# Performance work log

Hardware: AMD Instinct MI355X
Metric: run time of the kernel (lower is better)

The kernel has to match this reference:

```python
import jax, jax.numpy as jnp
import numpy as np

N = 50000      # nodes
E = 800000     # edges (avg degree 16)
DIN = 128      # input_dim
H = 256        # hidden_channels
DOUT = 64      # output_dim


def _glorot(k, shape):
    lim = float(np.sqrt(6.0 / (shape[0] + shape[1])))
    return jax.random.uniform(k, shape, jnp.float32, -lim, lim)


def setup_inputs() -> dict:
    key = jax.random.key(0)
    ks = jax.random.split(key, 10)
    return {
        "x": jax.random.normal(ks[0], (N, DIN), jnp.float32),
        "W1": _glorot(ks[3], (DIN, H)), "b1": jnp.zeros((H,), jnp.float32),
        "W2": _glorot(ks[4], (H, H)),   "b2": jnp.zeros((H,), jnp.float32),
        "L1w": _glorot(ks[5], (H, DIN)), "L1b": jnp.zeros((DIN,), jnp.float32),
        "L2w": _glorot(ks[6], (DIN, H)), "L2b": jnp.zeros((H,), jnp.float32),
        "W3": _glorot(ks[7], (H, DOUT)), "b3": jnp.zeros((DOUT,), jnp.float32),
        "adj": jax.random.randint(ks[1], (2, E), 0, N),
        "adj2": jax.random.randint(ks[2], (2, E), 0, N),
        "mode": 1,  # 1 -> 'l' (return logits); 0 -> softmax over classes
    }


def gcn_conv(x, edge_index, W, b):
    """PyG-style GCNConv: add self-loops, symmetric D^-1/2 A D^-1/2 norm,
    aggregate neighbor features, then (here fused) linear transform."""
    n = x.shape[0]
    loop = jnp.arange(n)
    src = jnp.concatenate([edge_index[0], loop])  # message sources (j)
    dst = jnp.concatenate([edge_index[1], loop])  # aggregation targets (i)
    deg = jax.ops.segment_sum(jnp.ones(src.shape[0], x.dtype), dst, num_segments=n)
    dinv = jax.lax.rsqrt(jnp.maximum(deg, 1.0))   # deg >= 1 due to self-loops
    norm = dinv[src] * dinv[dst]                  # [E+N]
    h = x @ W                                     # transform first (smaller of the two dims either way)
    msg = h[src] * norm[:, None]                  # gather + scale, [E+N, out]
    return jax.ops.segment_sum(msg, dst, num_segments=n) + b


def reference(x, W1, b1, W2, b2, L1w, L1b, L2w, L2b, W3, b3, adj, adj2, mode):
    h = jax.nn.relu(gcn_conv(x, adj, W1, b1))      # GCNConv(in->h) on adj
    h = jax.nn.relu(gcn_conv(h, adj2, W2, b2))     # GCNConv(h->h) on adj2
    h = jax.nn.relu(h @ L1w + L1b)                 # Linear(h->in)
    h = jax.nn.relu(h @ L2w + L2b)                 # Linear(in->h)
    out = gcn_conv(h, adj2, W3, b3)                # GCNConv(h->out) on adj2
    # dropout has p=0 -> identity
    return out if mode == 1 else jax.nn.softmax(out, axis=1)
```

## Files before the change

kernel.cpp:

```cpp
#include <hip/hip_runtime.h>
#include <hip/hip_bf16.h>
#include <cstdint>
#include <cstddef>

#define NNODES 50000
#define NEDGES 800000
#define D_IN   128
#define D_H    256
#define D_OUT  64
#define SCAN_BS 256
#define SCAN_NB ((NNODES + SCAN_BS - 1) / SCAN_BS)
#define BSH    9
#define BKN    (1 << BSH)
#define NBKT   ((NNODES + BKN - 1) / BKN)
#define MAXB   12288
#define CHUNK  2048

typedef __attribute__((ext_vector_type(8))) short bf16x8;
typedef __attribute__((ext_vector_type(4))) float f32x4;

__device__ __forceinline__ unsigned short f2bf(float f) {
    unsigned u = __builtin_bit_cast(unsigned, f);
    unsigned r = (u + 0x7FFFu + ((u >> 16) & 1u)) >> 16;
    return (unsigned short)r;
}
__device__ __forceinline__ float bf2f(unsigned short h) {
    unsigned u = ((unsigned)h) << 16;
    return __builtin_bit_cast(float, u);
}


__global__ __launch_bounds__(256) void k_bin(const int* __restrict__ adjA, const int* __restrict__ adjB,
                                             int* __restrict__ bcnt, unsigned* __restrict__ binned, int e) {
    __shared__ int h[NBKT], pfx[NBKT], put[NBKT], gbase[NBKT];
    __shared__ unsigned stage[CHUNK];
    const int g = blockIdx.y;
    const int* srcp = g ? adjB : adjA;
    const int* dstp = srcp + e;
    unsigned* outp = binned + (size_t)g * NBKT * MAXB;
    int* bc = bcnt + g * NBKT;
    const int tid = threadIdx.x;
    const int base = blockIdx.x * CHUNK;
    const int nrem = min(CHUNK, e - base);
    if (nrem <= 0) return;

    for (int t = tid; t < NBKT; t += 256) { h[t] = 0; put[t] = 0; }
    __syncthreads();

    unsigned pv[8];
    int bv[8];
    #pragma unroll
    for (int q = 0; q < 8; ++q) {
        int i = base + q * 256 + tid;
        bv[q] = -1;
        if (i < e) {
            int s = srcp[i];
            int d = dstp[i];
            pv[q] = ((unsigned)d << 16) | (unsigned)s;
            bv[q] = d >> BSH;
            atomicAdd(&h[bv[q]], 1);
        }
    }
    __syncthreads();
    if (tid == 0) {
        int r = 0;
        for (int k = 0; k < NBKT; ++k) { pfx[k] = r; r += h[k]; }
    }
    __syncthreads();
    #pragma unroll
    for (int q = 0; q < 8; ++q) {
        if (bv[q] >= 0) {
            int p = pfx[bv[q]] + atomicAdd(&put[bv[q]], 1);
            stage[p] = pv[q];
        }
    }
    __syncthreads();
    if (tid < NBKT && h[tid] > 0) gbase[tid] = atomicAdd(&bc[tid], h[tid]);
    __syncthreads();
    for (int idx = tid; idx < nrem; idx += 256) {
        unsigned v = stage[idx];
        int bb = v >> (16 + BSH);
        outp[(size_t)bb * MAXB + gbase[bb] + (idx - pfx[bb])] = v;
    }
}

__global__ __launch_bounds__(256) void k_hist_b(const unsigned* __restrict__ binned, const int* __restrict__ bcnt,
                                                int* __restrict__ cnt1, int* __restrict__ cnt2, int n) {
    __shared__ int lc[BKN];
    const int g = blockIdx.y;
    const int b = blockIdx.x;
    const unsigned* in = binned + (size_t)g * NBKT * MAXB + (size_t)b * MAXB;
    int* cnt = g ? cnt2 : cnt1;
    const int nb = bcnt[g * NBKT + b];
    const int base = b << BSH;
    for (int t = threadIdx.x; t < BKN; t += 256) lc[t] = 0;
    __syncthreads();
    for (int t = threadIdx.x; t < nb; t += 256) {
        unsigned v = in[t];
        atomicAdd(&lc[(v >> 16) & (BKN - 1)], 1);
    }
    __syncthreads();
    for (int t = threadIdx.x; t < BKN; t += 256)
        if (base + t < n) cnt[base + t] = lc[t];
}

__global__ __launch_bounds__(256) void k_scan_local2(const int* __restrict__ cnt1, const int* __restrict__ cnt2,
                                                     int* __restrict__ rp1, int* __restrict__ rp2,
                                                     int* __restrict__ bsum, int n) {
    __shared__ int s[SCAN_BS];
    const int g = blockIdx.x / SCAN_NB;
    const int blk = blockIdx.x - g * SCAN_NB;
    const int* cnt = g ? cnt2 : cnt1;
    int* rp = g ? rp2 : rp1;
    int t = threadIdx.x;
    int i = blk * SCAN_BS + t;
    int v = (i < n) ? cnt[i] : 0;
    int sum = v;
    s[t] = v;
    __syncthreads();
    #pragma unroll
    for (int off = 1; off < SCAN_BS; off <<= 1) {
        int u = (t >= off) ? s[t - off] : 0;
        __syncthreads();
        sum += u;
        s[t] = sum;
        __syncthreads();
    }
    if (i < n) rp[i] = sum - v;
    if (t == SCAN_BS - 1) bsum[blockIdx.x] = sum;
}

__global__ __launch_bounds__(256) void k_scan_top2(int* __restrict__ bsum) {
    __shared__ int s[SCAN_BS];
    int* b = bsum + blockIdx.x * SCAN_NB;
    int t = threadIdx.x;
    int v = (t < SCAN_NB) ? b[t] : 0;
    int sum = v;
    s[t] = v;
    __syncthreads();
    #pragma unroll
    for (int off = 1; off < SCAN_BS; off <<= 1) {
        int u = (t >= off) ? s[t - off] : 0;
        __syncthreads();
        sum += u;
        s[t] = sum;
        __syncthreads();
    }
    if (t < SCAN_NB) b[t] = sum - v;
}

__global__ __launch_bounds__(256) void k_scan_add2(int* __restrict__ rp1, int* __restrict__ rp2,
                                                   const int* __restrict__ bsum, int n) {
    const int g = blockIdx.x / SCAN_NB;
    const int blk = blockIdx.x - g * SCAN_NB;
    int* rp = g ? rp2 : rp1;
    int i = blk * SCAN_BS + threadIdx.x;
    if (i < n) rp[i] += bsum[blockIdx.x];
    if (i == 0) rp[n] = NEDGES;
}

__global__ void k_dinv2x(const int* __restrict__ cnt1, const int* __restrict__ cnt2,
                         float* __restrict__ dinv1, float* __restrict__ dinv2, int n) {
    int i = blockIdx.x * blockDim.x + threadIdx.x;
    if (i < n) dinv1[i] = rsqrtf((float)(cnt1[i] + 1));
    else if (i < 2 * n) dinv2[i - n] = rsqrtf((float)(cnt2[i - n] + 1));
}

__global__ __launch_bounds__(256) void k_scatter_lds(const unsigned* __restrict__ binned, const int* __restrict__ bcnt,
                                                     const int* __restrict__ rp1, const int* __restrict__ rp2,
                                                     int* __restrict__ col1, int* __restrict__ col2, int n) {
    __shared__ int lcur[BKN];
    __shared__ int srt[MAXB];
    const int g = blockIdx.y;
    const int b = blockIdx.x;
    const unsigned* in = binned + (size_t)g * NBKT * MAXB + (size_t)b * MAXB;
    const int* rp = g ? rp2 : rp1;
    int* col = g ? col2 : col1;
    const int base = b << BSH;
    const int rpb = rp[base];
    const int nb = bcnt[g * NBKT + b];
    for (int t = threadIdx.x; t < BKN; t += 256) {
        int node = base + t;
        lcur[t] = (node < n) ? rp[node] - rpb : 0;
    }
    __syncthreads();
    for (int t = threadIdx.x; t < nb; t += 256) {
        unsigned v = in[t];
        int pos = atomicAdd(&lcur[(v >> 16) & (BKN - 1)], 1);
        srt[pos] = (int)(v & 0xFFFFu);
    }
    __syncthreads();
    for (int t = threadIdx.x; t < nb; t += 256) col[rpb + t] = srt[t];
}


template<int F, bool PRESCALE>
__global__ __launch_bounds__(256) void k_quant(const float* __restrict__ in, const float* __restrict__ dscale,
                                               short* __restrict__ q, float* __restrict__ qs, int n) {
    constexpr int VPT = F / 64;
    const int lane = threadIdx.x & 63;
    const int i = blockIdx.x * 4 + (threadIdx.x >> 6);
    if (i >= n) return;
    float v[VPT];
    const float* p = in + (size_t)i * F + lane * VPT;
    if constexpr (VPT == 4) { float4 t = *(const float4*)p; v[0] = t.x; v[1] = t.y; v[2] = t.z; v[3] = t.w; }
    else if constexpr (VPT == 2) { float2 t = *(const float2*)p; v[0] = t.x; v[1] = t.y; }
    else v[0] = *p;
    if constexpr (PRESCALE) {
        float d = dscale[i];
        #pragma unroll
        for (int c = 0; c < VPT; ++c) v[c] *= d;
    }
    float m = 0.f;
    #pragma unroll
    for (int c = 0; c < VPT; ++c) m = fmaxf(m, fabsf(v[c]));
    #pragma unroll
    for (int off = 32; off > 0; off >>= 1) m = fmaxf(m, __shfl_xor(m, off));
    float inv = (m > 0.f) ? 32767.0f / m : 0.f;
    short* qp = q + (size_t)i * F + lane * VPT;
    if constexpr (VPT == 4) {
        short4 o;
        o.x = (short)__float2int_rn(v[0] * inv);
        o.y = (short)__float2int_rn(v[1] * inv);
        o.z = (short)__float2int_rn(v[2] * inv);
        o.w = (short)__float2int_rn(v[3] * inv);
        *(short4*)qp = o;
    } else if constexpr (VPT == 2) {
        short2 o;
        o.x = (short)__float2int_rn(v[0] * inv);
        o.y = (short)__float2int_rn(v[1] * inv);
        *(short2*)qp = o;
    } else {
        *qp = (short)__float2int_rn(v[0] * inv);
    }
    if (lane == 0) qs[i] = m * (1.0f / 32767.0f);
}


template<int F, int OUTM>
__global__ __launch_bounds__(256) void k_agg3(const short* __restrict__ q, const float* __restrict__ qs,
                                              const int* __restrict__ rp, const int* __restrict__ col,
                                              const float* __restrict__ dinv, const float* __restrict__ bias,
                                              void* __restrict__ outv, int n) {
    constexpr int VPT = F / 64;
    const int lane = threadIdx.x & 63;
    const int i = blockIdx.x * 4 + (threadIdx.x >> 6);
    if (i >= n) return;
    const short* ql = q + lane * VPT;
    float acc[VPT];
    #pragma unroll
    for (int c = 0; c < VPT; ++c) acc[c] = 0.f;

    int k = rp[i], end = rp[i + 1];

    auto body1 = [&](int j) {
        float s = qs[j];
        const short* pj = ql + (size_t)j * F;
        if constexpr (VPT == 4) {
            short4 v = *(const short4*)pj;
            acc[0] += s * (float)v.x; acc[1] += s * (float)v.y;
            acc[2] += s * (float)v.z; acc[3] += s * (float)v.w;
        } else if constexpr (VPT == 2) {
            short2 v = *(const short2*)pj;
            acc[0] += s * (float)v.x; acc[1] += s * (float)v.y;
        } else {
            acc[0] += s * (float)(*pj);
        }
    };

    body1(i);
    for (; k + 4 <= end; k += 4) {
        int j0 = col[k], j1 = col[k + 1], j2 = col[k + 2], j3 = col[k + 3];
        float s0 = qs[j0], s1 = qs[j1], s2 = qs[j2], s3 = qs[j3];
        if constexpr (VPT == 4) {
            short4 v0 = *(const short4*)(ql + (size_t)j0 * F);
            short4 v1 = *(const short4*)(ql + (size_t)j1 * F);
            short4 v2 = *(const short4*)(ql + (size_t)j2 * F);
            short4 v3 = *(const short4*)(ql + (size_t)j3 * F);
            acc[0] += s0 * (float)v0.x + s1 * (float)v1.x + s2 * (float)v2.x + s3 * (float)v3.x;
            acc[1] += s0 * (float)v0.y + s1 * (float)v1.y + s2 * (float)v2.y + s3 * (float)v3.y;
            acc[2] += s0 * (float)v0.z + s1 * (float)v1.z + s2 * (float)v2.z + s3 * (float)v3.z;
            acc[3] += s0 * (float)v0.w + s1 * (float)v1.w + s2 * (float)v2.w + s3 * (float)v3.w;
        } else if constexpr (VPT == 2) {
            short2 v0 = *(const short2*)(ql + (size_t)j0 * F);
            short2 v1 = *(const short2*)(ql + (size_t)j1 * F);
            short2 v2 = *(const short2*)(ql + (size_t)j2 * F);
            short2 v3 = *(const short2*)(ql + (size_t)j3 * F);
            acc[0] += s0 * (float)v0.x + s1 * (float)v1.x + s2 * (float)v2.x + s3 * (float)v3.x;
            acc[1] += s0 * (float)v0.y + s1 * (float)v1.y + s2 * (float)v2.y + s3 * (float)v3.y;
        } else {
            float v0 = (float)ql[(size_t)j0 * F];
            float v1 = (float)ql[(size_t)j1 * F];
            float v2 = (float)ql[(size_t)j2 * F];
            float v3 = (float)ql[(size_t)j3 * F];
            acc[0] += s0 * v0 + s1 * v1 + s2 * v2 + s3 * v3;
        }
    }
    for (; k < end; ++k) body1(col[k]);

    float di = dinv[i];
    if constexpr (OUTM == 0) {
        unsigned short* o = (unsigned short*)outv + (size_t)i * 2 * F + lane * VPT;
        #pragma unroll
        for (int c = 0; c < VPT; ++c) {
            float val = acc[c] * di;
            unsigned short h = f2bf(val);
            unsigned short l = f2bf(val - bf2f(h));
            o[c] = h;
            o[F + c] = l;
        }
    } else {
        float* o = (float*)outv + (size_t)i * F + lane * VPT;
        #pragma unroll
        for (int c = 0; c < VPT; ++c) o[c] = acc[c] * di + bias[lane * VPT + c];
    }
}


__device__ __forceinline__ void wconv1(const float* __restrict__ W, unsigned short* __restrict__ Th,
                                       unsigned short* __restrict__ Tl, int idx, int K, int Nc) {
    int k = idx / Nc, n = idx - k * Nc;
    float v = W[idx];
    unsigned short h = f2bf(v);
    unsigned short l = f2bf(v - bf2f(h));
    Th[(size_t)n * K + k] = h;
    Tl[(size_t)n * K + k] = l;
}

__global__ void k_wconv_all(const float* W1, const float* W2, const float* L1w, const float* L2w, const float* W3,
                            unsigned short* W1h, unsigned short* W1l, unsigned short* W2h, unsigned short* W2l,
                            unsigned short* L1h, unsigned short* L1l, unsigned short* L2h, unsigned short* L2l,
                            unsigned short* W3h, unsigned short* W3l) {
    int idx = blockIdx.x * blockDim.x + threadIdx.x;
    if (idx < 32768)        wconv1(W1, W1h, W1l, idx, D_IN, D_H);
    else if (idx < 98304)   wconv1(W2, W2h, W2l, idx - 32768, D_H, D_H);
    else if (idx < 131072)  wconv1(L1w, L1h, L1l, idx - 98304, D_H, D_IN);
    else if (idx < 163840)  wconv1(L2w, L2h, L2l, idx - 131072, D_IN, D_H);
    else if (idx < 180224)  wconv1(W3, W3h, W3l, idx - 163840, D_H, D_OUT);
}


template<bool RELU, bool BIAS, int OUTM>
__global__ __launch_bounds__(256) void k_gemm3(const unsigned short* __restrict__ Ahl,
        const unsigned short* __restrict__ Bth, const unsigned short* __restrict__ Btl,
        const float* __restrict__ bias, const float* __restrict__ dscale,
        void* __restrict__ Cv, int M, int K, int Nc, int ncb) {
    constexpr int PAD = 66;
    __shared__ unsigned short As_h[128][PAD];
    __shared__ unsigned short As_l[128][PAD];
    __shared__ unsigned short Bs_h[64][PAD];
    __shared__ unsigned short Bs_l[64][PAD];

    const int nwg = gridDim.x;
    const int b = blockIdx.x;
    const int q8 = nwg >> 3, r8 = nwg & 7;
    const int xcd = b & 7;
    const int swz = (xcd < r8 ? xcd * (q8 + 1) : r8 * (q8 + 1) + (xcd - r8) * q8) + (b >> 3);
    const int row0 = (swz / ncb) * 128;
    const int col0 = (swz % ncb) * 64;

    const int tid = threadIdx.x;
    const int lane = tid & 63;
    const int wv = tid >> 6;

    f32x4 acc[2][4];
    #pragma unroll
    for (int m = 0; m < 2; ++m)
        #pragma unroll
        for (int n = 0; n < 4; ++n) acc[m][n] = (f32x4)(0.f);

    const int srow = tid >> 1;
    const int skh = (tid & 1) * 32;
    int arow = row0 + srow;
    if (arow >= M) arow = M - 1;
    const unsigned short* aph = Ahl + (size_t)arow * 2 * K + skh;
    const unsigned short* apl = aph + K;

    const int bn = tid >> 2;
    const int bko = (tid & 3) * 16;
    const unsigned short* bph = Bth + (size_t)(col0 + bn) * K + bko;
    const unsigned short* bpl = Btl + (size_t)(col0 + bn) * K + bko;

    const int fr = lane & 15;
    const int fk = (lane >> 4) * 8;

    const int nk = K >> 6;
    for (int kt = 0; kt < nk; ++kt) {
        uint4 ah0 = *(const uint4*)(aph + kt * 64);
        uint4 ah1 = *(const uint4*)(aph + kt * 64 + 8);
        uint4 ah2 = *(const uint4*)(aph + kt * 64 + 16);
        uint4 ah3 = *(const uint4*)(aph + kt * 64 + 24);
        uint4 al0 = *(const uint4*)(apl + kt * 64);
        uint4 al1 = *(const uint4*)(apl + kt * 64 + 8);
        uint4 al2 = *(const uint4*)(apl + kt * 64 + 16);
        uint4 al3 = *(const uint4*)(apl + kt * 64 + 24);
        uint4 bh0 = *(const uint4*)(bph + kt * 64);
        uint4 bh1 = *(const uint4*)(bph + kt * 64 + 8);
        uint4 bl0 = *(const uint4*)(bpl + kt * 64);
        uint4 bl1 = *(const uint4*)(bpl + kt * 64 + 8);

        __syncthreads();

        *(uint4*)&As_h[srow][skh] = ah0;
        *(uint4*)&As_h[srow][skh + 8] = ah1;
        *(uint4*)&As_h[srow][skh + 16] = ah2;
        *(uint4*)&As_h[srow][skh + 24] = ah3;
        *(uint4*)&As_l[srow][skh] = al0;
        *(uint4*)&As_l[srow][skh + 8] = al1;
        *(uint4*)&As_l[srow][skh + 16] = al2;
        *(uint4*)&As_l[srow][skh + 24] = al3;
        *(uint4*)&Bs_h[bn][bko] = bh0;
        *(uint4*)&Bs_h[bn][bko + 8] = bh1;
        *(uint4*)&Bs_l[bn][bko] = bl0;
        *(uint4*)&Bs_l[bn][bko + 8] = bl1;

        __syncthreads();

        #pragma unroll
        for (int ks = 0; ks < 2; ++ks) {
            const int ko = ks * 32 + fk;
            bf16x8 ah[2], al[2], bh[4], bl[4];
            #pragma unroll
            for (int m = 0; m < 2; ++m) {
                ah[m] = *(const bf16x8*)&As_h[wv * 32 + m * 16 + fr][ko];
                al[m] = *(const bf16x8*)&As_l[wv * 32 + m * 16 + fr][ko];
            }
            #pragma unroll
            for (int n = 0; n < 4; ++n) {
                bh[n] = *(const bf16x8*)&Bs_h[n * 16 + fr][ko];
                bl[n] = *(const bf16x8*)&Bs_l[n * 16 + fr][ko];
            }
            #pragma unroll
            for (int m = 0; m < 2; ++m)
                #pragma unroll
                for (int n = 0; n < 4; ++n) {
                    acc[m][n] = __builtin_amdgcn_mfma_f32_16x16x32_bf16(ah[m], bh[n], acc[m][n], 0, 0, 0);
                    acc[m][n] = __builtin_amdgcn_mfma_f32_16x16x32_bf16(ah[m], bl[n], acc[m][n], 0, 0, 0);
                    acc[m][n] = __builtin_amdgcn_mfma_f32_16x16x32_bf16(al[m], bh[n], acc[m][n], 0, 0, 0);
                }
        }
    }

    float bv[4];
    #pragma unroll
    for (int n = 0; n < 4; ++n) bv[n] = BIAS ? bias[col0 + n * 16 + fr] : 0.f;
    const int rbase = row0 + wv * 32 + (lane >> 4) * 4;
    #pragma unroll
    for (int m = 0; m < 2; ++m) {
        #pragma unroll
        for (int j = 0; j < 4; ++j) {
            const int r = rbase + m * 16 + j;
            if (r >= M) continue;
            float ds = 1.f;
            if constexpr (OUTM == 1) ds = dscale[r];
            #pragma unroll
            for (int n = 0; n < 4; ++n) {
                const int c = col0 + n * 16 + fr;
                float o = acc[m][n][j] + bv[n];
                if constexpr (RELU) o = fmaxf(o, 0.f);
                if constexpr (OUTM == 1) {
                    ((float*)Cv)[(size_t)r * Nc + c] = o * ds;
                } else {
                    unsigned short h = f2bf(o);
                    unsigned short l = f2bf(o - bf2f(h));
                    unsigned short* C2 = (unsigned short*)Cv + (size_t)r * 2 * Nc + c;
                    C2[0] = h;
                    C2[Nc] = l;
                }
            }
        }
    }
}


__global__ __launch_bounds__(256) void k_softmax(float* __restrict__ out, const int* __restrict__ mode, int n) {
    if (*mode == 1) return;
    int lane = threadIdx.x & 63;
    int i = blockIdx.x * 4 + (threadIdx.x >> 6);
    if (i >= n) return;
    float v = out[(size_t)i * 64 + lane];
    float m = v;
    #pragma unroll
    for (int off = 32; off > 0; off >>= 1) m = fmaxf(m, __shfl_xor(m, off));
    float e = __expf(v - m);
    float s = e;
    #pragma unroll
    for (int off = 32; off > 0; off >>= 1) s += __shfl_xor(s, off);
    out[(size_t)i * 64 + lane] = e / s;
}


extern "C" void kernel_launch(void* const* d_in, const int* in_sizes, int n_in,
                              void* d_out, int out_size, void* d_ws, size_t ws_size,
                              hipStream_t stream) {
    const float* x   = (const float*)d_in[0];
    const float* W1  = (const float*)d_in[1];
    const float* b1  = (const float*)d_in[2];
    const float* W2  = (const float*)d_in[3];
    const float* b2  = (const float*)d_in[4];
    const float* L1w = (const float*)d_in[5];
    const float* L1b = (const float*)d_in[6];
    const float* L2w = (const float*)d_in[7];
    const float* L2b = (const float*)d_in[8];
    const float* W3  = (const float*)d_in[9];
    const float* b3  = (const float*)d_in[10];
    const int* adj   = (const int*)d_in[11];
    const int* adj2  = (const int*)d_in[12];
    const int* mode  = (const int*)d_in[13];
    float* out = (float*)d_out;

    char* ws = (char*)d_ws;
    auto alloc = [&](size_t bytes) {
        char* p = ws;
        ws += (bytes + 255) & ~(size_t)255;
        return p;
    };
    char*  bufA  = alloc((size_t)NNODES * 256 * 4);
    char*  bufB  = alloc((size_t)NNODES * 256 * 4);
    int*   rp1   = (int*)alloc((NNODES + 1) * 4);
    int*   col1  = (int*)alloc((size_t)NEDGES * 4);
    int*   rp2   = (int*)alloc((NNODES + 1) * 4);
    int*   col2  = (int*)alloc((size_t)NEDGES * 4);
    float* dinv1 = (float*)alloc(NNODES * 4);
    float* dinv2 = (float*)alloc(NNODES * 4);
    int*   cnt1  = (int*)alloc((size_t)NNODES * 4);
    int*   cnt2  = (int*)alloc((size_t)NNODES * 4);
    int*   bsum  = (int*)alloc(2 * SCAN_NB * 4);
    int*   bcnt  = (int*)alloc(2 * NBKT * 4);
    float* qs    = (float*)alloc(NNODES * 4);
    unsigned short* W1h = (unsigned short*)alloc(D_IN * D_H * 2);
    unsigned short* W1l = (unsigned short*)alloc(D_IN * D_H * 2);
    unsigned short* W2h = (unsigned short*)alloc(D_H * D_H * 2);
    unsigned short* W2l = (unsigned short*)alloc(D_H * D_H * 2);
    unsigned short* L1h = (unsigned short*)alloc(D_H * D_IN * 2);
    unsigned short* L1l = (unsigned short*)alloc(D_H * D_IN * 2);
    unsigned short* L2h = (unsigned short*)alloc(D_IN * D_H * 2);
    unsigned short* L2l = (unsigned short*)alloc(D_IN * D_H * 2);
    unsigned short* W3h = (unsigned short*)alloc(D_H * D_OUT * 2);
    unsigned short* W3l = (unsigned short*)alloc(D_H * D_OUT * 2);
    unsigned* binned = (unsigned*)bufA;

    const int AGB = (NNODES + 3) / 4;
    const int MT = (NNODES + 127) / 128;
    const int BINB = (NEDGES + CHUNK - 1) / CHUNK;

    k_wconv_all<<<(180224 + 255) / 256, 256, 0, stream>>>(W1, W2, L1w, L2w, W3,
        W1h, W1l, W2h, W2l, L1h, L1l, L2h, L2l, W3h, W3l);

    hipMemsetAsync(bcnt, 0, 2 * NBKT * 4, stream);
    k_bin<<<dim3(BINB, 2), 256, 0, stream>>>(adj, adj2, bcnt, binned, NEDGES);
    k_hist_b<<<dim3(NBKT, 2), 256, 0, stream>>>(binned, bcnt, cnt1, cnt2, NNODES);
    k_scan_local2<<<2 * SCAN_NB, 256, 0, stream>>>(cnt1, cnt2, rp1, rp2, bsum, NNODES);
    k_scan_top2<<<2, 256, 0, stream>>>(bsum);
    k_scan_add2<<<2 * SCAN_NB, 256, 0, stream>>>(rp1, rp2, bsum, NNODES);
    k_dinv2x<<<(2 * NNODES + 255) / 256, 256, 0, stream>>>(cnt1, cnt2, dinv1, dinv2, NNODES);
    k_scatter_lds<<<dim3(NBKT, 2), 256, 0, stream>>>(binned, bcnt, rp1, rp2, col1, col2, NNODES);

    k_quant<128, true><<<AGB, 256, 0, stream>>>(x, dinv1, (short*)bufA, qs, NNODES);
    k_agg3<128, 0><<<AGB, 256, 0, stream>>>((const short*)bufA, qs, rp1, col1, dinv1, nullptr, bufB, NNODES);
    k_gemm3<true, true, 1><<<MT * 4, 256, 0, stream>>>(
        (const unsigned short*)bufB, W1h, W1l, b1, dinv2, bufA, NNODES, D_IN, D_H, 4);
    k_quant<256, false><<<AGB, 256, 0, stream>>>((const float*)bufA, nullptr, (short*)bufB, qs, NNODES);
    k_agg3<256, 0><<<AGB, 256, 0, stream>>>((const short*)bufB, qs, rp2, col2, dinv2, nullptr, bufA, NNODES);
    k_gemm3<true, true, 2><<<MT * 4, 256, 0, stream>>>(
        (const unsigned short*)bufA, W2h, W2l, b2, nullptr, bufB, NNODES, D_H, D_H, 4);
    k_gemm3<true, true, 2><<<MT * 2, 256, 0, stream>>>(
        (const unsigned short*)bufB, L1h, L1l, L1b, nullptr, bufA, NNODES, D_H, D_IN, 2);
    k_gemm3<true, true, 2><<<MT * 4, 256, 0, stream>>>(
        (const unsigned short*)bufA, L2h, L2l, L2b, nullptr, bufB, NNODES, D_IN, D_H, 4);
    k_gemm3<false, false, 1><<<MT * 1, 256, 0, stream>>>(
        (const unsigned short*)bufB, W3h, W3l, nullptr, dinv2, bufA, NNODES, D_H, D_OUT, 1);
    k_quant<64, false><<<AGB, 256, 0, stream>>>((const float*)bufA, nullptr, (short*)bufB, qs, NNODES);
    k_agg3<64, 1><<<AGB, 256, 0, stream>>>((const short*)bufB, qs, rp2, col2, dinv2, b3, out, NNODES);
    k_softmax<<<AGB, 256, 0, stream>>>(out, mode, NNODES);
}
```

Measured before the change: 359.8 us.

## Split aggregation into 32-column slices with 4 edge groups per wave

Replaces the per-node aggregation kernel with one where each block handles a 32-feature column slice. Each wave is split into four 16-lane groups that walk different edges in parallel, and the partial sums are combined with cross-lane shuffles. Block indices are interleaved so the 8 blocks sharing a group of rows run next to each other, which is meant to improve cache locality for the gathered rows. This adds more parallelism per node and shortens the per-lane dependency chain, at the cost of narrower 4-byte gathers per lane, more redundant reads of col and qs, and a shuffle reduction.

```diff
diff --git a/kernel.cpp b/kernel.cpp
--- a/kernel.cpp
+++ b/kernel.cpp
@@ -238,81 +238,52 @@
 
 
 template<int F, int OUTM>
-__global__ __launch_bounds__(256) void k_agg3(const short* __restrict__ q, const float* __restrict__ qs,
+__global__ __launch_bounds__(256) void k_agg4(const short* __restrict__ q, const float* __restrict__ qs,
                                               const int* __restrict__ rp, const int* __restrict__ col,
                                               const float* __restrict__ dinv, const float* __restrict__ bias,
                                               void* __restrict__ outv, int n) {
-    constexpr int VPT = F / 64;
+    constexpr int NSL = F / 32;
+    constexpr int REP = 8 / NSL;
+    const int blk = blockIdx.x;
+    const int v8 = blk & 7;
+    const int sl = v8 % NSL;
+    const int r  = v8 / NSL;
+    const int chunk = (blk >> 3) * REP + r;
+    const int wv = threadIdx.x >> 6;
     const int lane = threadIdx.x & 63;
-    const int i = blockIdx.x * 4 + (threadIdx.x >> 6);
+    const int grp = lane >> 4;
+    const int gl = lane & 15;
+    const int i = chunk * 4 + wv;
     if (i >= n) return;
-    const short* ql = q + lane * VPT;
-    float acc[VPT];
-    #pragma unroll
-    for (int c = 0; c < VPT; ++c) acc[c] = 0.f;
-
-    int k = rp[i], end = rp[i + 1];
-
-    auto body1 = [&](int j) {
+    const int c0 = sl * 32 + gl * 2;
+    const short* qc = q + c0;
+
+    float a0 = 0.f, a1 = 0.f;
+    const int beg = rp[i], end = rp[i + 1];
+    for (int idx = beg - 1 + grp; idx < end; idx += 4) {
+        int j = (idx < beg) ? i : col[idx];
         float s = qs[j];
-        const short* pj = ql + (size_t)j * F;
-        if constexpr (VPT == 4) {
-            short4 v = *(const short4*)pj;
-            acc[0] += s * (float)v.x; acc[1] += s * (float)v.y;
-            acc[2] += s * (float)v.z; acc[3] += s * (float)v.w;
-        } else if constexpr (VPT == 2) {
-            short2 v = *(const short2*)pj;
-            acc[0] += s * (float)v.x; acc[1] += s * (float)v.y;
-        } else {
-            acc[0] += s * (float)(*pj);
-        }
-    };
-
-    body1(i);
-    for (; k + 4 <= end; k += 4) {
-        int j0 = col[k], j1 = col[k + 1], j2 = col[k + 2], j3 = col[k + 3];
-        float s0 = qs[j0], s1 = qs[j1], s2 = qs[j2], s3 = qs[j3];
-        if constexpr (VPT == 4) {
-            short4 v0 = *(const short4*)(ql + (size_t)j0 * F);
-            short4 v1 = *(const short4*)(ql + (size_t)j1 * F);
-            short4 v2 = *(const short4*)(ql + (size_t)j2 * F);
-            short4 v3 = *(const short4*)(ql + (size_t)j3 * F);
-            acc[0] += s0 * (float)v0.x + s1 * (float)v1.x + s2 * (float)v2.x + s3 * (float)v3.x;
-            acc[1] += s0 * (float)v0.y + s1 * (float)v1.y + s2 * (float)v2.y + s3 * (float)v3.y;
-            acc[2] += s0 * (float)v0.z + s1 * (float)v1.z + s2 * (float)v2.z + s3 * (float)v3.z;
-            acc[3] += s0 * (float)v0.w + s1 * (float)v1.w + s2 * (float)v2.w + s3 * (float)v3.w;
-        } else if constexpr (VPT == 2) {
-            short2 v0 = *(const short2*)(ql + (size_t)j0 * F);
-            short2 v1 = *(const short2*)(ql + (size_t)j1 * F);
-            short2 v2 = *(const short2*)(ql + (size_t)j2 * F);
-            short2 v3 = *(const short2*)(ql + (size_t)j3 * F);
-            acc[0] += s0 * (float)v0.x + s1 * (float)v1.x + s2 * (float)v2.x + s3 * (float)v3.x;
-            acc[1] += s0 * (float)v0.y + s1 * (float)v1.y + s2 * (float)v2.y + s3 * (float)v3.y;
-        } else {
-            float v0 = (float)ql[(size_t)j0 * F];
-            float v1 = (float)ql[(size_t)j1 * F];
-            float v2 = (float)ql[(size_t)j2 * F];
-            float v3 = (float)ql[(size_t)j3 * F];
-            acc[0] += s0 * v0 + s1 * v1 + s2 * v2 + s3 * v3;
-        }
-    }
-    for (; k < end; ++k) body1(col[k]);
-
-    float di = dinv[i];
+        short2 v = *(const short2*)(qc + (size_t)j * F);
+        a0 += s * (float)v.x;
+        a1 += s * (float)v.y;
+    }
+    a0 += __shfl_xor(a0, 16); a1 += __shfl_xor(a1, 16);
+    a0 += __shfl_xor(a0, 32); a1 += __shfl_xor(a1, 32);
+    if (grp != 0) return;
+
+    const float di = dinv[i];
+    const float v0 = a0 * di, v1 = a1 * di;
     if constexpr (OUTM == 0) {
-        unsigned short* o = (unsigned short*)outv + (size_t)i * 2 * F + lane * VPT;
-        #pragma unroll
-        for (int c = 0; c < VPT; ++c) {
-            float val = acc[c] * di;
-            unsigned short h = f2bf(val);
-            unsigned short l = f2bf(val - bf2f(h));
-            o[c] = h;
-            o[F + c] = l;
-        }
+        unsigned short* o = (unsigned short*)outv + (size_t)i * 2 * F + c0;
+        unsigned short h0 = f2bf(v0), h1 = f2bf(v1);
+        ushort2 hh; hh.x = h0; hh.y = h1;
+        ushort2 ll; ll.x = f2bf(v0 - bf2f(h0)); ll.y = f2bf(v1 - bf2f(h1));
+        *(ushort2*)o = hh;
+        *(ushort2*)(o + F) = ll;
     } else {
-        float* o = (float*)outv + (size_t)i * F + lane * VPT;
-        #pragma unroll
-        for (int c = 0; c < VPT; ++c) o[c] = acc[c] * di + bias[lane * VPT + c];
+        float* o = (float*)outv + (size_t)i * F + c0;
+        float2 ov; ov.x = v0 + bias[c0]; ov.y = v1 + bias[c0 + 1];
+        *(float2*)o = ov;
     }
 }
 
@@ -543,6 +514,9 @@
     const int AGB = (NNODES + 3) / 4;
     const int MT = (NNODES + 127) / 128;
     const int BINB = (NEDGES + CHUNK - 1) / CHUNK;
+    const int AG256 = 12500 * 8;
+    const int AG128 = ((12500 + 1) / 2) * 8;
+    const int AG64  = ((12500 + 3) / 4) * 8;
 
     k_wconv_all<<<(180224 + 255) / 256, 256, 0, stream>>>(W1, W2, L1w, L2w, W3,
         W1h, W1l, W2h, W2l, L1h, L1l, L2h, L2l, W3h, W3l);
@@ -557,11 +531,11 @@
     k_scatter_lds<<<dim3(NBKT, 2), 256, 0, stream>>>(binned, bcnt, rp1, rp2, col1, col2, NNODES);
 
     k_quant<128, true><<<AGB, 256, 0, stream>>>(x, dinv1, (short*)bufA, qs, NNODES);
-    k_agg3<128, 0><<<AGB, 256, 0, stream>>>((const short*)bufA, qs, rp1, col1, dinv1, nullptr, bufB, NNODES);
+    k_agg4<128, 0><<<AG128, 256, 0, stream>>>((const short*)bufA, qs, rp1, col1, dinv1, nullptr, bufB, NNODES);
     k_gemm3<true, true, 1><<<MT * 4, 256, 0, stream>>>(
         (const unsigned short*)bufB, W1h, W1l, b1, dinv2, bufA, NNODES, D_IN, D_H, 4);
     k_quant<256, false><<<AGB, 256, 0, stream>>>((const float*)bufA, nullptr, (short*)bufB, qs, NNODES);
-    k_agg3<256, 0><<<AGB, 256, 0, stream>>>((const short*)bufB, qs, rp2, col2, dinv2, nullptr, bufA, NNODES);
+    k_agg4<256, 0><<<AG256, 256, 0, stream>>>((const short*)bufB, qs, rp2, col2, dinv2, nullptr, bufA, NNODES);
     k_gemm3<true, true, 2><<<MT * 4, 256, 0, stream>>>(
         (const unsigned short*)bufA, W2h, W2l, b2, nullptr, bufB, NNODES, D_H, D_H, 4);
     k_gemm3<true, true, 2><<<MT * 2, 256, 0, stream>>>(
@@ -571,6 +545,6 @@
     k_gemm3<false, false, 1><<<MT * 1, 256, 0, stream>>>(
         (const unsigned short*)bufB, W3h, W3l, nullptr, dinv2, bufA, NNODES, D_H, D_OUT, 1);
     k_quant<64, false><<<AGB, 256, 0, stream>>>((const float*)bufA, nullptr, (short*)bufB, qs, NNODES);
-    k_agg3<64, 1><<<AGB, 256, 0, stream>>>((const short*)bufB, qs, rp2, col2, dinv2, b3, out, NNODES);
+    k_agg4<64, 1><<<AG64, 256, 0, stream>>>((const short*)bufB, qs, rp2, col2, dinv2, b3, out, NNODES);
     k_softmax<<<AGB, 256, 0, stream>>>(out, mode, NNODES);
 }
```

New measurement: 604.7 us. +68.1%, slower.

## Fuse CSR build into bucket scan plus per-bucket histogram/scan/scatter kernel

Applied to the files above, without the earlier changes.

Replaces the per-node histogram, three-kernel global scan, dinv kernel and scatter kernel with two launches. A tiny single-block kernel scans the 98 bucket counts per graph, and a per-bucket kernel then builds the local histogram, does an in-LDS scan, and writes row pointers, dinv and sorted columns. This removes several launches and the global passes over the count arrays. The serial per-bucket scan runs on one thread per graph, which is cheap at this bucket count.

```diff
diff --git a/kernel.cpp b/kernel.cpp
--- a/kernel.cpp
+++ b/kernel.cpp
@@ -8,8 +8,6 @@
 #define D_IN   128
 #define D_H    256
 #define D_OUT  64
-#define SCAN_BS 256
-#define SCAN_NB ((NNODES + SCAN_BS - 1) / SCAN_BS)
 #define BSH    9
 #define BKN    (1 << BSH)
 #define NBKT   ((NNODES + BKN - 1) / BKN)
@@ -84,113 +82,80 @@
     }
 }
 
-__global__ __launch_bounds__(256) void k_hist_b(const unsigned* __restrict__ binned, const int* __restrict__ bcnt,
-                                                int* __restrict__ cnt1, int* __restrict__ cnt2, int n) {
+__global__ void k_bktscan(const int* __restrict__ bcnt, int* __restrict__ bbase,
+                          int* __restrict__ rp1, int* __restrict__ rp2) {
+    __shared__ int s[2][NBKT];
+    int t = threadIdx.x;
+    if (t < NBKT) s[0][t] = bcnt[t];
+    else if (t < 2 * NBKT) s[1][t - NBKT] = bcnt[t];
+    __syncthreads();
+    if (t < 2) {
+        int r = 0;
+        for (int k = 0; k < NBKT; ++k) { int v = s[t][k]; s[t][k] = r; r += v; }
+    }
+    __syncthreads();
+    if (t < NBKT) bbase[t] = s[0][t];
+    else if (t < 2 * NBKT) bbase[t] = s[1][t - NBKT];
+    if (t == 0) { rp1[NNODES] = NEDGES; rp2[NNODES] = NEDGES; }
+}
+
+__global__ __launch_bounds__(256) void k_csr_bucket(const unsigned* __restrict__ binned,
+                                                    const int* __restrict__ bcnt, const int* __restrict__ bbase,
+                                                    int* __restrict__ rp1, int* __restrict__ rp2,
+                                                    float* __restrict__ dinv1, float* __restrict__ dinv2,
+                                                    int* __restrict__ col1, int* __restrict__ col2, int n) {
     __shared__ int lc[BKN];
-    const int g = blockIdx.y;
-    const int b = blockIdx.x;
-    const unsigned* in = binned + (size_t)g * NBKT * MAXB + (size_t)b * MAXB;
-    int* cnt = g ? cnt2 : cnt1;
-    const int nb = bcnt[g * NBKT + b];
-    const int base = b << BSH;
-    for (int t = threadIdx.x; t < BKN; t += 256) lc[t] = 0;
-    __syncthreads();
-    for (int t = threadIdx.x; t < nb; t += 256) {
-        unsigned v = in[t];
-        atomicAdd(&lc[(v >> 16) & (BKN - 1)], 1);
-    }
-    __syncthreads();
-    for (int t = threadIdx.x; t < BKN; t += 256)
-        if (base + t < n) cnt[base + t] = lc[t];
-}
-
-__global__ __launch_bounds__(256) void k_scan_local2(const int* __restrict__ cnt1, const int* __restrict__ cnt2,
-                                                     int* __restrict__ rp1, int* __restrict__ rp2,
-                                                     int* __restrict__ bsum, int n) {
-    __shared__ int s[SCAN_BS];
-    const int g = blockIdx.x / SCAN_NB;
-    const int blk = blockIdx.x - g * SCAN_NB;
-    const int* cnt = g ? cnt2 : cnt1;
-    int* rp = g ? rp2 : rp1;
-    int t = threadIdx.x;
-    int i = blk * SCAN_BS + t;
-    int v = (i < n) ? cnt[i] : 0;
-    int sum = v;
-    s[t] = v;
-    __syncthreads();
-    #pragma unroll
-    for (int off = 1; off < SCAN_BS; off <<= 1) {
-        int u = (t >= off) ? s[t - off] : 0;
-        __syncthreads();
-        sum += u;
-        s[t] = sum;
-        __syncthreads();
-    }
-    if (i < n) rp[i] = sum - v;
-    if (t == SCAN_BS - 1) bsum[blockIdx.x] = sum;
-}
-
-__global__ __launch_bounds__(256) void k_scan_top2(int* __restrict__ bsum) {
-    __shared__ int s[SCAN_BS];
-    int* b = bsum + blockIdx.x * SCAN_NB;
-    int t = threadIdx.x;
-    int v = (t < SCAN_NB) ? b[t] : 0;
-    int sum = v;
-    s[t] = v;
-    __syncthreads();
-    #pragma unroll
-    for (int off = 1; off < SCAN_BS; off <<= 1) {
-        int u = (t >= off) ? s[t - off] : 0;
-        __syncthreads();
-        sum += u;
-        s[t] = sum;
-        __syncthreads();
-    }
-    if (t < SCAN_NB) b[t] = sum - v;
-}
-
-__global__ __launch_bounds__(256) void k_scan_add2(int* __restrict__ rp1, int* __restrict__ rp2,
-                                                   const int* __restrict__ bsum, int n) {
-    const int g = blockIdx.x / SCAN_NB;
-    const int blk = blockIdx.x - g * SCAN_NB;
-    int* rp = g ? rp2 : rp1;
-    int i = blk * SCAN_BS + threadIdx.x;
-    if (i < n) rp[i] += bsum[blockIdx.x];
-    if (i == 0) rp[n] = NEDGES;
-}
-
-__global__ void k_dinv2x(const int* __restrict__ cnt1, const int* __restrict__ cnt2,
-                         float* __restrict__ dinv1, float* __restrict__ dinv2, int n) {
-    int i = blockIdx.x * blockDim.x + threadIdx.x;
-    if (i < n) dinv1[i] = rsqrtf((float)(cnt1[i] + 1));
-    else if (i < 2 * n) dinv2[i - n] = rsqrtf((float)(cnt2[i - n] + 1));
-}
-
-__global__ __launch_bounds__(256) void k_scatter_lds(const unsigned* __restrict__ binned, const int* __restrict__ bcnt,
-                                                     const int* __restrict__ rp1, const int* __restrict__ rp2,
-                                                     int* __restrict__ col1, int* __restrict__ col2, int n) {
-    __shared__ int lcur[BKN];
+    __shared__ int loff[BKN];
+    __shared__ int ps[256];
     __shared__ int srt[MAXB];
     const int g = blockIdx.y;
     const int b = blockIdx.x;
     const unsigned* in = binned + (size_t)g * NBKT * MAXB + (size_t)b * MAXB;
-    const int* rp = g ? rp2 : rp1;
+    int* rp = g ? rp2 : rp1;
+    float* dinv = g ? dinv2 : dinv1;
     int* col = g ? col2 : col1;
-    const int base = b << BSH;
-    const int rpb = rp[base];
     const int nb = bcnt[g * NBKT + b];
-    for (int t = threadIdx.x; t < BKN; t += 256) {
-        int node = base + t;
-        lcur[t] = (node < n) ? rp[node] - rpb : 0;
-    }
-    __syncthreads();
-    for (int t = threadIdx.x; t < nb; t += 256) {
+    const int base0 = bbase[g * NBKT + b];
+    const int nodebase = b << BSH;
+    const int tid = threadIdx.x;
+
+    for (int t = tid; t < BKN; t += 256) lc[t] = 0;
+    __syncthreads();
+    for (int t = tid; t < nb; t += 256)
+        atomicAdd(&lc[(in[t] >> 16) & (BKN - 1)], 1);
+    __syncthreads();
+    int c0 = lc[2 * tid], c1 = lc[2 * tid + 1];
+    int pair = c0 + c1;
+    int sum = pair;
+    ps[tid] = pair;
+    __syncthreads();
+    #pragma unroll
+    for (int off = 1; off < 256; off <<= 1) {
+        int u = (tid >= off) ? ps[tid - off] : 0;
+        __syncthreads();
+        sum += u;
+        ps[tid] = sum;
+        __syncthreads();
+    }
+    int excl = sum - pair;
+    loff[2 * tid] = excl;
+    loff[2 * tid + 1] = excl + c0;
+    __syncthreads();
+    for (int t = tid; t < BKN; t += 256) {
+        int node = nodebase + t;
+        if (node < n) {
+            rp[node] = base0 + loff[t];
+            dinv[node] = rsqrtf((float)(lc[t] + 1));
+        }
+    }
+    __syncthreads();
+    for (int t = tid; t < nb; t += 256) {
         unsigned v = in[t];
-        int pos = atomicAdd(&lcur[(v >> 16) & (BKN - 1)], 1);
+        int pos = atomicAdd(&loff[(v >> 16) & (BKN - 1)], 1);
         srt[pos] = (int)(v & 0xFFFFu);
     }
     __syncthreads();
-    for (int t = threadIdx.x; t < nb; t += 256) col[rpb + t] = srt[t];
+    for (int t = tid; t < nb; t += 256) col[base0 + t] = srt[t];
 }
 
 
@@ -523,10 +488,8 @@
     int*   col2  = (int*)alloc((size_t)NEDGES * 4);
     float* dinv1 = (float*)alloc(NNODES * 4);
     float* dinv2 = (float*)alloc(NNODES * 4);
-    int*   cnt1  = (int*)alloc((size_t)NNODES * 4);
-    int*   cnt2  = (int*)alloc((size_t)NNODES * 4);
-    int*   bsum  = (int*)alloc(2 * SCAN_NB * 4);
     int*   bcnt  = (int*)alloc(2 * NBKT * 4);
+    int*   bbase = (int*)alloc(2 * NBKT * 4);
     float* qs    = (float*)alloc(NNODES * 4);
     unsigned short* W1h = (unsigned short*)alloc(D_IN * D_H * 2);
     unsigned short* W1l = (unsigned short*)alloc(D_IN * D_H * 2);
@@ -549,12 +512,9 @@
 
     hipMemsetAsync(bcnt, 0, 2 * NBKT * 4, stream);
     k_bin<<<dim3(BINB, 2), 256, 0, stream>>>(adj, adj2, bcnt, binned, NEDGES);
-    k_hist_b<<<dim3(NBKT, 2), 256, 0, stream>>>(binned, bcnt, cnt1, cnt2, NNODES);
-    k_scan_local2<<<2 * SCAN_NB, 256, 0, stream>>>(cnt1, cnt2, rp1, rp2, bsum, NNODES);
-    k_scan_top2<<<2, 256, 0, stream>>>(bsum);
-    k_scan_add2<<<2 * SCAN_NB, 256, 0, stream>>>(rp1, rp2, bsum, NNODES);
-    k_dinv2x<<<(2 * NNODES + 255) / 256, 256, 0, stream>>>(cnt1, cnt2, dinv1, dinv2, NNODES);
-    k_scatter_lds<<<dim3(NBKT, 2), 256, 0, stream>>>(binned, bcnt, rp1, rp2, col1, col2, NNODES);
+    k_bktscan<<<1, 256, 0, stream>>>(bcnt, bbase, rp1, rp2);
+    k_csr_bucket<<<dim3(NBKT, 2), 256, 0, stream>>>(binned, bcnt, bbase, rp1, rp2,
+                                                    dinv1, dinv2, col1, col2, NNODES);
 
     k_quant<128, true><<<AGB, 256, 0, stream>>>(x, dinv1, (short*)bufA, qs, NNODES);
     k_agg3<128, 0><<<AGB, 256, 0, stream>>>((const short*)bufA, qs, rp1, col1, dinv1, nullptr, bufB, NNODES);
```

After: 351.9 us. 1.02x faster.
